# Kernel optimization log

Hardware: AMD Instinct MI355X
Metric: run time of the kernel (lower is better)

## Reference

```python
import jax, jax.numpy as jnp
import numpy as np

PI = 3.1415926
CHAINS = [[0, 2, 5, 8, 11], [0, 1, 4, 7, 10], [0, 3, 6, 9, 12, 15], [9, 14, 17, 19, 21], [9, 13, 16, 18, 20]]
NUM_JOINTS = 22
CTX = 512
B = 131072


def setup_inputs() -> dict:
    key = jax.random.key(0)
    k_ctx, k_w0, k_b0, k_w, k_b = jax.random.split(key, 5)
    context_vec = jax.random.normal(k_ctx, (B, CTX), dtype=jnp.float32)
    # root linear: context_size -> 3
    W0 = jax.random.normal(k_w0, (CTX, 3), dtype=jnp.float32) * 0.02
    b0 = jax.random.normal(k_b0, (3,), dtype=jnp.float32) * 0.02
    # non-root linears: (context_size + 3) -> 3, stacked per joint index (row 0 unused)
    W = jax.random.normal(k_w, (NUM_JOINTS, CTX + 3, 3), dtype=jnp.float32) * 0.02
    b = jax.random.normal(k_b, (NUM_JOINTS, 3), dtype=jnp.float32) * 0.02
    return {"context_vec": context_vec, "W0": W0, "b0": b0, "W": W, "b": b}


def reference(context_vec, W0, b0, W, b):
    # Sequential per-joint tiny linears along kinematic chains (do_all_parent=False):
    # each child consumes [context, parent_joint(3)] -> 3, then tanh * PI.
    joints = [None] * NUM_JOINTS
    joints[0] = jnp.tanh(context_vec @ W0 + b0) * PI  # [B, 3]
    for chain in CHAINS:
        for j in range(1, len(chain)):
            jid = chain[j]
            inp = jnp.concatenate([context_vec, joints[chain[j - 1]]], axis=-1)  # [B, CTX+3]
            joints[jid] = jnp.tanh(inp @ W[jid] + b[jid]) * PI
    return jnp.concatenate(joints, axis=-1)  # [B, 3*NUM_JOINTS]
```

## Files before the change

kernel.cpp:

```cpp
#include <hip/hip_runtime.h>
#include <cstdint>
#include <cstddef>


#define CTXD 512
#define NCOL 66
#define KT   16
#define NT   5
#define RPB  128
#define LDS_STRIDE 67

typedef __attribute__((ext_vector_type(8))) short  short8;
typedef __attribute__((ext_vector_type(4))) float  f32x4;

__device__ __forceinline__ unsigned short f2bf(float x) {
  unsigned u = __float_as_uint(x);
  return (unsigned short)((u + 0x7FFFu + ((u >> 16) & 1u)) >> 16);
}

__device__ __forceinline__ unsigned cvt2(float a, float b) {
  unsigned r;
  asm("v_cvt_pk_bf16_f32 %0, %1, %2" : "=v"(r) : "v"(a), "v"(b));
  return r;
}

__device__ __forceinline__ float tanhpi(float x) {
  float t = exp2f(x * 2.885390081777927f);
  return 3.1415926f - 6.2831852f * __builtin_amdgcn_rcpf(t + 1.0f);
}

__global__ void prep_wfrag(const float* __restrict__ W0,
                           const float* __restrict__ W,
                           unsigned short* __restrict__ wf) {
  int idx = blockIdx.x * blockDim.x + threadIdx.x;
  if (idx >= KT * NT * 64 * 8) return;
  int j    = idx & 7;
  int lane = (idx >> 3) & 63;
  int rest = idx >> 9;
  int nt   = rest % NT;
  int kt   = rest / NT;
  int k    = kt * 32 + (lane >> 4) * 8 + j;
  int col  = nt * 16 + (lane & 15);
  float v = 0.f;
  if (col < 3)          v = W0[k * 3 + col];
  else if (col < NCOL)  v = W[(col / 3) * (515 * 3) + k * 3 + (col % 3)];
  wf[idx] = f2bf(v);
}

__global__ __launch_bounds__(256, 4) void hdl_main(
    const float* __restrict__ ctx,
    const float* __restrict__ b0,
    const float* __restrict__ W,
    const float* __restrict__ bflat,
    const unsigned short* __restrict__ wf,
    float* __restrict__ out)
{
  __shared__ float smem[RPB * LDS_STRIDE];

  const int tid  = threadIdx.x;
  const int lane = tid & 63;
  const int wave = tid >> 6;
  const int r16  = lane & 15;
  const int kg   = lane >> 4;
  const long blockRow = (long)blockIdx.x * RPB;

  f32x4 acc[2][NT] = {};

  float bias[NT];
#pragma unroll
  for (int n = 0; n < NT; ++n) {
    int col = n * 16 + r16;
    bias[n] = (col < 3) ? b0[col] : ((col < NCOL) ? bflat[col] : 0.f);
  }

  float* stage = smem + wave * 2048;
  const float* srcBase =
      ctx + (blockRow + wave * 32 + (lane >> 3)) * (long)CTXD
          + (((lane & 7) ^ (lane >> 3)) << 2);

#define ISSUE_GLL(ktv, buf)                                                    \
  {                                                                            \
    _Pragma("unroll")                                                          \
    for (int j = 0; j < 4; ++j) {                                              \
      const float* s = srcBase + (size_t)(j * 8) * CTXD + (ktv) * 32;          \
      __builtin_amdgcn_global_load_lds(                                        \
          (const __attribute__((address_space(1))) void*)s,                    \
          (__attribute__((address_space(3))) void*)((buf) + j * 256),          \
          16, 0, 0);                                                           \
    }                                                                          \
  }

  ISSUE_GLL(0, stage)

#pragma unroll
  for (int kt = 0; kt < KT; ++kt) {
    const float* cur = stage + (kt & 1) * 1024;
    float* nxt = stage + ((kt + 1) & 1) * 1024;

    short8 bfr[NT];
#pragma unroll
    for (int n = 0; n < NT; ++n)
      bfr[n] = *(const short8*)(wf + (size_t)((kt * NT + n) * 64 + lane) * 8);

    if (kt < KT - 1) {
      ISSUE_GLL(kt + 1, nxt)
      asm volatile("s_waitcnt vmcnt(4)" ::: "memory");
    } else {
      asm volatile("s_waitcnt vmcnt(0)" ::: "memory");
    }

#pragma unroll
    for (int m = 0; m < 2; ++m) {
      const int row = m * 16 + r16;
      const float* rbase = cur + row * 32;
      const int rx = r16 & 7;
      float4 f0 = *(const float4*)(rbase + ((((kg * 2)     ) ^ rx) << 2));
      float4 f1 = *(const float4*)(rbase + ((((kg * 2) + 1 ) ^ rx) << 2));
      union { short8 s; unsigned u[4]; } A;
      A.u[0] = cvt2(f0.x, f0.y);
      A.u[1] = cvt2(f0.z, f0.w);
      A.u[2] = cvt2(f1.x, f1.y);
      A.u[3] = cvt2(f1.z, f1.w);
#pragma unroll
      for (int n = 0; n < NT; ++n)
        acc[m][n] = __builtin_amdgcn_mfma_f32_16x16x32_bf16(
            A.s, bfr[n], acc[m][n], 0, 0, 0);
    }
  }

  __syncthreads();

#pragma unroll
  for (int m = 0; m < 2; ++m) {
#pragma unroll
    for (int n = 0; n < NT; ++n) {
      int col = n * 16 + r16;
      if (col < NCOL) {
        int rb = wave * 32 + m * 16 + kg * 4;
#pragma unroll
        for (int q = 0; q < 4; ++q)
          smem[(rb + q) * LDS_STRIDE + col] = acc[m][n][q] + bias[n];
      }
    }
  }
  __syncthreads();

  if (tid < RPB) {
    float* row = smem + tid * LDS_STRIDE;
    float J[22][3];
#pragma unroll
    for (int cc = 0; cc < 3; ++cc) J[0][cc] = tanhpi(row[cc]);

    constexpr int EP[21] = {0,2,5,8, 0,1,4,7, 0,3,6,9,12, 9,14,17,19, 9,13,16,18};
    constexpr int EC[21] = {2,5,8,11, 1,4,7,10, 3,6,9,12,15, 14,17,19,21, 13,16,18,20};
#pragma unroll
    for (int e = 0; e < 21; ++e) {
      const int p  = EP[e];
      const int ch = EC[e];
      const float* wp = W + ch * 1545 + 1536;
#pragma unroll
      for (int cc = 0; cc < 3; ++cc) {
        float s = row[3 * ch + cc];
        s += J[p][0] * wp[cc] + J[p][1] * wp[3 + cc] + J[p][2] * wp[6 + cc];
        J[ch][cc] = tanhpi(s);
      }
    }
#pragma unroll
    for (int jj = 0; jj < 22; ++jj)
#pragma unroll
      for (int cc = 0; cc < 3; ++cc) row[3 * jj + cc] = J[jj][cc];
  }
  __syncthreads();

  const size_t outBase = (size_t)blockRow * NCOL;
  for (int i = tid; i < RPB * NCOL; i += 256) {
    int r = i / NCOL;
    int cc = i - r * NCOL;
    out[outBase + i] = smem[r * LDS_STRIDE + cc];
  }
}

extern "C" void kernel_launch(void* const* d_in, const int* in_sizes, int n_in,
                              void* d_out, int out_size, void* d_ws, size_t ws_size,
                              hipStream_t stream) {
  const float* ctx  = (const float*)d_in[0];
  const float* W0   = (const float*)d_in[1];
  const float* b0   = (const float*)d_in[2];
  const float* W    = (const float*)d_in[3];
  const float* bfl  = (const float*)d_in[4];
  unsigned short* wf = (unsigned short*)d_ws;

  int prep_elems = KT * NT * 64 * 8;
  hipLaunchKernelGGL(prep_wfrag, dim3((prep_elems + 255) / 256), dim3(256), 0,
                     stream, W0, W, wf);

  int nrows = out_size / NCOL;
  hipLaunchKernelGGL(hdl_main, dim3(nrows / RPB), dim3(256), 0,
                     stream, ctx, b0, W, bfl, wf, (float*)d_out);
}
```

Before: 63.73 us.

## Fuse weight-fragment prep into main kernel with global flag handshake

Moves the bf16 weight-fragment preparation into the first 160 blocks of the main kernel and drops the separate prep launch. Other blocks start their first context prefetch, then spin on a global atomic counter until every prep block has published. It also sets a cache-policy bit on the global-to-LDS loads and defers the bias loads until after the MMA loop. This removes one kernel launch and its gap, but it depends on the prep blocks being scheduled before waiting blocks fill the device, adds a memset launch, and makes early blocks wait on a spin loop.

```diff
diff --git a/kernel.cpp b/kernel.cpp
--- a/kernel.cpp
+++ b/kernel.cpp
@@ -9,6 +9,8 @@
 #define NT   5
 #define RPB  128
 #define LDS_STRIDE 67
+#define PREP_BLOCKS 160
+#define WF_ELEMS (KT * NT * 64 * 8)
 
 typedef __attribute__((ext_vector_type(8))) short  short8;
 typedef __attribute__((ext_vector_type(4))) float  f32x4;
@@ -29,30 +31,14 @@
   return 3.1415926f - 6.2831852f * __builtin_amdgcn_rcpf(t + 1.0f);
 }
 
-__global__ void prep_wfrag(const float* __restrict__ W0,
-                           const float* __restrict__ W,
-                           unsigned short* __restrict__ wf) {
-  int idx = blockIdx.x * blockDim.x + threadIdx.x;
-  if (idx >= KT * NT * 64 * 8) return;
-  int j    = idx & 7;
-  int lane = (idx >> 3) & 63;
-  int rest = idx >> 9;
-  int nt   = rest % NT;
-  int kt   = rest / NT;
-  int k    = kt * 32 + (lane >> 4) * 8 + j;
-  int col  = nt * 16 + (lane & 15);
-  float v = 0.f;
-  if (col < 3)          v = W0[k * 3 + col];
-  else if (col < NCOL)  v = W[(col / 3) * (515 * 3) + k * 3 + (col % 3)];
-  wf[idx] = f2bf(v);
-}
-
-__global__ __launch_bounds__(256, 4) void hdl_main(
+__global__ __launch_bounds__(256, 4) void hdl_fused(
     const float* __restrict__ ctx,
+    const float* __restrict__ W0,
     const float* __restrict__ b0,
     const float* __restrict__ W,
     const float* __restrict__ bflat,
-    const unsigned short* __restrict__ wf,
+    unsigned short* __restrict__ wf,
+    unsigned int* __restrict__ flag,
     float* __restrict__ out)
 {
   __shared__ float smem[RPB * LDS_STRIDE];
@@ -64,13 +50,20 @@
   const int kg   = lane >> 4;
   const long blockRow = (long)blockIdx.x * RPB;
 
-  f32x4 acc[2][NT] = {};
-
-  float bias[NT];
-#pragma unroll
-  for (int n = 0; n < NT; ++n) {
-    int col = n * 16 + r16;
-    bias[n] = (col < 3) ? b0[col] : ((col < NCOL) ? bflat[col] : 0.f);
+  if (blockIdx.x < PREP_BLOCKS) {
+    int idx  = blockIdx.x * 256 + tid;
+    int j    = idx & 7;
+    int l2   = (idx >> 3) & 63;
+    int rest = idx >> 9;
+    int nt   = rest % NT;
+    int kt   = rest / NT;
+    int k    = kt * 32 + (l2 >> 4) * 8 + j;
+    int col  = nt * 16 + (l2 & 15);
+    float v = 0.f;
+    if (col < 3)          v = W0[k * 3 + col];
+    else if (col < NCOL)  v = W[(col / 3) * 1545 + k * 3 + (col % 3)];
+    wf[idx] = f2bf(v);
+    __threadfence();
   }
 
   float* stage = smem + wave * 2048;
@@ -86,11 +79,26 @@
       __builtin_amdgcn_global_load_lds(                                        \
           (const __attribute__((address_space(1))) void*)s,                    \
           (__attribute__((address_space(3))) void*)((buf) + j * 256),          \
-          16, 0, 0);                                                           \
+          16, 0, 2 );            \
     }                                                                          \
   }
 
   ISSUE_GLL(0, stage)
+
+  asm volatile("" ::: "memory");
+  __builtin_amdgcn_s_barrier();
+  if (tid == 0) {
+    if (blockIdx.x < PREP_BLOCKS)
+      __hip_atomic_fetch_add(flag, 1u, __ATOMIC_RELEASE,
+                             __HIP_MEMORY_SCOPE_AGENT);
+    while (__hip_atomic_load(flag, __ATOMIC_ACQUIRE,
+                             __HIP_MEMORY_SCOPE_AGENT) < PREP_BLOCKS)
+      __builtin_amdgcn_s_sleep(8);
+  }
+  __builtin_amdgcn_s_barrier();
+  asm volatile("" ::: "memory");
+
+  f32x4 acc[2][NT] = {};
 
 #pragma unroll
   for (int kt = 0; kt < KT; ++kt) {
@@ -114,8 +122,8 @@
       const int row = m * 16 + r16;
       const float* rbase = cur + row * 32;
       const int rx = r16 & 7;
-      float4 f0 = *(const float4*)(rbase + ((((kg * 2)     ) ^ rx) << 2));
-      float4 f1 = *(const float4*)(rbase + ((((kg * 2) + 1 ) ^ rx) << 2));
+      float4 f0 = *(const float4*)(rbase + ((((kg * 2)    ) ^ rx) << 2));
+      float4 f1 = *(const float4*)(rbase + ((((kg * 2) + 1) ^ rx) << 2));
       union { short8 s; unsigned u[4]; } A;
       A.u[0] = cvt2(f0.x, f0.y);
       A.u[1] = cvt2(f0.z, f0.w);
@@ -130,6 +138,13 @@
 
   __syncthreads();
 
+  float bias[NT];
+#pragma unroll
+  for (int n = 0; n < NT; ++n) {
+    int col = n * 16 + r16;
+    bias[n] = (col < 3) ? b0[col] : ((col < NCOL) ? bflat[col] : 0.f);
+  }
+
 #pragma unroll
   for (int m = 0; m < 2; ++m) {
 #pragma unroll
@@ -174,7 +189,7 @@
 
   const size_t outBase = (size_t)blockRow * NCOL;
   for (int i = tid; i < RPB * NCOL; i += 256) {
-    int r = i / NCOL;
+    int r  = i / NCOL;
     int cc = i - r * NCOL;
     out[outBase + i] = smem[r * LDS_STRIDE + cc];
   }
@@ -189,12 +204,11 @@
   const float* W    = (const float*)d_in[3];
   const float* bfl  = (const float*)d_in[4];
   unsigned short* wf = (unsigned short*)d_ws;
-
-  int prep_elems = KT * NT * 64 * 8;
-  hipLaunchKernelGGL(prep_wfrag, dim3((prep_elems + 255) / 256), dim3(256), 0,
-                     stream, W0, W, wf);
+  unsigned int* flag = (unsigned int*)((char*)d_ws + WF_ELEMS * 2);
+
+  hipMemsetAsync((void*)flag, 0, sizeof(unsigned int), stream);
 
   int nrows = out_size / NCOL;
-  hipLaunchKernelGGL(hdl_main, dim3(nrows / RPB), dim3(256), 0,
-                     stream, ctx, b0, W, bfl, wf, (float*)d_out);
-}
+  hipLaunchKernelGGL(hdl_fused, dim3(nrows / RPB), dim3(256), 0,
+                     stream, ctx, W0, b0, W, bfl, wf, flag, (float*)d_out);
+}
```

Result: slower. 138.2 us (+116.8%).
